# Kernel tuning notes

Hardware: AMD Instinct MI355X
Metric: run time of the kernel (lower is better)

The kernel has to match this reference:

```python
import jax, jax.numpy as jnp
import numpy as np

N = 50000
E = 800000
D_IN = 128
D_OUT = 64


def setup_inputs() -> dict:
    key = jax.random.key(0)
    ks = jax.random.split(key, 8)
    x = jax.random.normal(ks[0], (N, D_IN), dtype=jnp.float32)
    edge_index = jax.random.randint(ks[1], (2, E), 0, N, dtype=jnp.int64)
    s = 1.0 / np.sqrt(D_IN)
    # PyG SAGEConv: lin_l (applied to aggregated neighbors, has bias), lin_r (root, no bias)
    w1_l = jax.random.uniform(ks[2], (D_IN, D_IN), jnp.float32, -s, s)
    b1 = jnp.zeros((D_IN,), jnp.float32)
    w1_r = jax.random.uniform(ks[3], (D_IN, D_IN), jnp.float32, -s, s)
    w2_l = jax.random.uniform(ks[4], (D_IN, D_OUT), jnp.float32, -s, s)
    b2 = jnp.zeros((D_OUT,), jnp.float32)
    w2_r = jax.random.uniform(ks[5], (D_IN, D_OUT), jnp.float32, -s, s)
    return {"x": x, "edge_index": edge_index, "w1_l": w1_l, "b1": b1,
            "w1_r": w1_r, "w2_l": w2_l, "b2": b2, "w2_r": w2_r}


def _sage_conv(x, src, dst, w_l, b_l, w_r):
    # mean-aggregate source features at destination nodes
    msg_sum = jax.ops.segment_sum(x[src], dst, num_segments=N)  # [N, d]
    cnt = jax.ops.segment_sum(jnp.ones((src.shape[0],), x.dtype), dst, num_segments=N)
    mean = msg_sum / jnp.maximum(cnt, 1.0)[:, None]
    out = mean @ w_l + b_l + x @ w_r
    # L2 normalize (normalize=True)
    norm = jnp.linalg.norm(out, axis=-1, keepdims=True)
    return out / jnp.maximum(norm, 1e-12)


def reference(x, edge_index, w1_l, b1, w1_r, w2_l, b2, w2_r):
    src, dst = edge_index[0], edge_index[1]
    h = _sage_conv(x, src, dst, w1_l, b1, w1_r)
    h = _sage_conv(h, src, dst, w2_l, b2, w2_r)
    return h
```

## Files before the change

### kernel.cpp

```cpp
#include <hip/hip_runtime.h>
#include <math.h>

#define NN 50000
#define EE 800000
#define NB 196
#define CAP 6144

typedef __attribute__((ext_vector_type(8))) short bf16x8;
typedef __attribute__((ext_vector_type(16))) float f32x16;
typedef __attribute__((ext_vector_type(4))) unsigned short us4;

__device__ inline unsigned short bf16_rne(float f) {
    union { float f; unsigned u; } a; a.f = f;
    unsigned u = a.u;
    u += 0x7fff + ((u >> 16) & 1);
    return (unsigned short)(u >> 16);
}
__device__ inline float bf16_lo(unsigned v) {
    union { unsigned u; float f; } a; a.u = v << 16;
    return a.f;
}
__device__ inline float bf16_hi(unsigned v) {
    union { unsigned u; float f; } a; a.u = v & 0xffff0000u;
    return a.f;
}

__global__ void prep_all_kernel(const float* __restrict__ w1l, const float* __restrict__ w1r,
                                const float* __restrict__ w2l, const float* __restrict__ w2r,
                                unsigned short* __restrict__ wt1, unsigned short* __restrict__ wt2,
                                unsigned short* __restrict__ y1pad, unsigned short* __restrict__ y2pad,
                                int* __restrict__ bcur) {
    int idx = blockIdx.x * 256 + threadIdx.x;
    if (idx < 32768) {
        int n = idx >> 7, k = idx & 127;
        float v = (n < 128) ? w1l[(size_t)k * 128 + n] : w1r[(size_t)k * 128 + (n - 128)];
        wt1[idx] = bf16_rne(v);
    } else if (idx < 49152) {
        int j = idx - 32768;
        int n = j >> 7, k = j & 127;
        float v = (n < 64) ? w2l[(size_t)k * 64 + n] : w2r[(size_t)k * 64 + (n - 64)];
        wt2[j] = bf16_rne(v);
    } else {
        int j = idx - 49152;
        if (j < 128) y1pad[j] = 0;
        else if (j < 192) y2pad[j - 128] = 0;
        else if (j < 192 + NB) bcur[j - 192] = 0;
    }
}

__global__ __launch_bounds__(1024) void bin_kernel(
        const int* __restrict__ src, const int* __restrict__ dst,
        int* __restrict__ gcur, int* __restrict__ rec, int E) {
    __shared__ int hist[NB];
    __shared__ int cur[NB];
    const int t = threadIdx.x;
    const int per = (E + gridDim.x - 1) / gridDim.x;
    const int lo = blockIdx.x * per;
    const int hi = min(lo + per, E);

    for (int i = t; i < NB; i += 1024) hist[i] = 0;
    __syncthreads();
    for (int e = lo + t; e < hi; e += 1024)
        atomicAdd(&hist[dst[e] >> 8], 1);
    __syncthreads();
    for (int i = t; i < NB; i += 1024)
        cur[i] = atomicAdd(&gcur[i], hist[i]);
    __syncthreads();
    for (int e = lo + t; e < hi; e += 1024) {
        int d = dst[e], s = src[e];
        int cb = d >> 8;
        int p = atomicAdd(&cur[cb], 1);
        if (p < CAP) rec[(size_t)cb * CAP + p] = ((d & 255) << 16) | s;
    }
}

__global__ __launch_bounds__(256) void place_kernel(
        const int* __restrict__ rec, const int* __restrict__ bcur,
        int* __restrict__ rowoff, unsigned short* __restrict__ csr, int n) {
    __shared__ int bscan[256];
    __shared__ int cnt[256];
    __shared__ int cur[256];
    __shared__ unsigned short sorted[CAP];
    const int cb = blockIdx.x, t = threadIdx.x;

    bscan[t] = (t < NB) ? bcur[t] : 0;
    __syncthreads();
    for (int ofs = 1; ofs < 256; ofs <<= 1) {
        int v = bscan[t];
        int a = (t >= ofs) ? bscan[t - ofs] : 0;
        __syncthreads();
        bscan[t] = v + a;
        __syncthreads();
    }
    const int base = (cb == 0) ? 0 : bscan[cb - 1];

    int m = bcur[cb]; if (m > CAP) m = CAP;
    const int* r = rec + (size_t)cb * CAP;

    cnt[t] = 0;
    __syncthreads();
    for (int i = t; i < m; i += 256) atomicAdd(&cnt[r[i] >> 16], 1);
    __syncthreads();
    int orig = cnt[t];
    for (int ofs = 1; ofs < 256; ofs <<= 1) {
        int v = cnt[t];
        int a = (t >= ofs) ? cnt[t - ofs] : 0;
        __syncthreads();
        cnt[t] = v + a;
        __syncthreads();
    }
    int excl = cnt[t] - orig;
    int node = cb * 256 + t;
    if (node < n) rowoff[node] = base + excl;
    if (node == n - 1) rowoff[n] = base + cnt[t];
    cur[t] = excl;
    __syncthreads();
    for (int i = t; i < m; i += 256) {
        int rr = r[i];
        int pos = atomicAdd(&cur[rr >> 16], 1);
        sorted[pos] = (unsigned short)(rr & 0xffff);
    }
    __syncthreads();
    for (int i = t; i < m; i += 256) csr[base + i] = sorted[i];
}

template <int CO, bool BF16IN>
__global__ __launch_bounds__(256) void transform_mfma_kernel(
        const void* __restrict__ xin, const unsigned short* __restrict__ wt,
        const float* __restrict__ bias, unsigned short* __restrict__ ybuf,
        unsigned short* __restrict__ rbuf, int n) {
    constexpr int HALF = CO / 2;
    constexpr int LDW = 136;
    __shared__ unsigned short Xs[64][LDW];
    __shared__ unsigned short Ws[64][LDW];

    const int t = threadIdx.x;
    const int node0 = blockIdx.x * 64;
    const int gy = blockIdx.y;

    if (BF16IN) {
        const unsigned short* xb = (const unsigned short*)xin;
        for (int e = t; e < 64 * 16; e += 256) {
            int nd = e >> 4, c8 = e & 15;
            int node = node0 + nd;
            int4 v = (node < n) ? ((const int4*)(xb + (size_t)node * 128))[c8]
                                : make_int4(0, 0, 0, 0);
            *(int4*)&Xs[nd][c8 * 8] = v;
        }
    } else {
        const float* xf = (const float*)xin;
        for (int e = t; e < 64 * 32; e += 256) {
            int nd = e >> 5, c4 = e & 31;
            int node = node0 + nd;
            float4 v = (node < n) ? ((const float4*)xf)[(size_t)node * 32 + c4]
                                  : make_float4(0.f, 0.f, 0.f, 0.f);
            us4 p;
            p.x = bf16_rne(v.x); p.y = bf16_rne(v.y); p.z = bf16_rne(v.z); p.w = bf16_rne(v.w);
            *(us4*)&Xs[nd][c4 * 4] = p;
        }
    }
    for (int e = t; e < 64 * 16; e += 256) {
        int nd = e >> 4, c8 = e & 15;
        int4 v = ((const int4*)(wt + ((size_t)(gy * 64 + nd)) * 128))[c8];
        *(int4*)&Ws[nd][c8 * 8] = v;
    }
    __syncthreads();

    const int lane = t & 63, wave = t >> 6;
    const int wm = (wave & 1) * 32, wn = (wave >> 1) * 32;
    const int ml = wm + (lane & 31);
    const int nl = wn + (lane & 31);
    const int koff = (lane >> 5) * 8;

    f32x16 acc;
#pragma unroll
    for (int r = 0; r < 16; r++) acc[r] = 0.f;

#pragma unroll
    for (int kk = 0; kk < 8; kk++) {
        bf16x8 a = *(const bf16x8*)&Xs[ml][kk * 16 + koff];
        bf16x8 b = *(const bf16x8*)&Ws[nl][kk * 16 + koff];
        acc = __builtin_amdgcn_mfma_f32_32x32x16_bf16(a, b, acc, 0, 0, 0);
    }

    const int col = gy * 64 + wn + (lane & 31);
    if (col < HALF) {
#pragma unroll
        for (int r = 0; r < 16; r++) {
            int row = (r & 3) + 8 * (r >> 2) + 4 * (lane >> 5);
            int node = node0 + wm + row;
            if (node < n) ybuf[(size_t)node * HALF + col] = bf16_rne(acc[r]);
        }
    } else {
        const float bj = bias[col - HALF];
#pragma unroll
        for (int r = 0; r < 16; r++) {
            int row = (r & 3) + 8 * (r >> 2) + 4 * (lane >> 5);
            int node = node0 + wm + row;
            if (node < n) rbuf[(size_t)node * HALF + (col - HALF)] = bf16_rne(acc[r] + bj);
        }
    }
}

__global__ __launch_bounds__(256) void gather128_kernel(
        const unsigned short* __restrict__ y, const unsigned short* __restrict__ rrb,
        const int* __restrict__ rowoff, const unsigned short* __restrict__ csr,
        unsigned short* __restrict__ out, int n) {
    const int wave = threadIdx.x >> 6;
    const int lane = threadIdx.x & 63;
    const int node = blockIdx.x * 4 + wave;
    if (node >= n) return;
    const int g = lane >> 4;
    const int q = lane & 15;

    const int off = rowoff[node];
    const int end = rowoff[node + 1];
    const int deg = end - off;

    float acc[8];
#pragma unroll
    for (int j = 0; j < 8; j++) acc[j] = 0.f;

    for (int k0 = 0; k0 < deg; k0 += 8) {
        int kk0 = off + k0 + g;
        int kk1 = off + k0 + 4 + g;
        int i0 = (kk0 < end) ? (int)csr[kk0] : n;
        int i1 = (kk1 < end) ? (int)csr[kk1] : n;
        uint4 v0 = *(const uint4*)(y + (size_t)i0 * 128 + q * 8);
        uint4 v1 = *(const uint4*)(y + (size_t)i1 * 128 + q * 8);
        const unsigned* u0 = (const unsigned*)&v0;
        const unsigned* u1 = (const unsigned*)&v1;
#pragma unroll
        for (int i = 0; i < 4; i++) {
            acc[2 * i]     += bf16_lo(u0[i]) + bf16_lo(u1[i]);
            acc[2 * i + 1] += bf16_hi(u0[i]) + bf16_hi(u1[i]);
        }
    }
#pragma unroll
    for (int j = 0; j < 8; j++) {
        acc[j] += __shfl_xor(acc[j], 16, 64);
        acc[j] += __shfl_xor(acc[j], 32, 64);
    }
    const float im = 1.0f / fmaxf((float)deg, 1.0f);
    uint4 rv = *(const uint4*)(rrb + (size_t)node * 128 + q * 8);
    const unsigned* ru = (const unsigned*)&rv;
    float v[8];
    float ss = 0.f;
#pragma unroll
    for (int i = 0; i < 4; i++) {
        v[2 * i]     = acc[2 * i] * im     + bf16_lo(ru[i]);
        v[2 * i + 1] = acc[2 * i + 1] * im + bf16_hi(ru[i]);
    }
#pragma unroll
    for (int j = 0; j < 8; j++) ss += v[j] * v[j];
#pragma unroll
    for (int m = 8; m >= 1; m >>= 1) ss += __shfl_xor(ss, m, 64);
    const float rn = 1.0f / fmaxf(sqrtf(ss), 1e-12f);
    if (g == 0) {
        uint4 pk;
        unsigned* pu = (unsigned*)&pk;
#pragma unroll
        for (int i = 0; i < 4; i++)
            pu[i] = (unsigned)bf16_rne(v[2 * i] * rn) |
                    ((unsigned)bf16_rne(v[2 * i + 1] * rn) << 16);
        *(uint4*)(out + (size_t)node * 128 + q * 8) = pk;
    }
}

__global__ __launch_bounds__(256) void gather64_kernel(
        const unsigned short* __restrict__ y, const unsigned short* __restrict__ rrb,
        const int* __restrict__ rowoff, const unsigned short* __restrict__ csr,
        float* __restrict__ out, int n) {
    const int wave = threadIdx.x >> 6;
    const int lane = threadIdx.x & 63;
    const int node = blockIdx.x * 4 + wave;
    if (node >= n) return;
    const int g = lane >> 3;
    const int q = lane & 7;

    const int off = rowoff[node];
    const int end = rowoff[node + 1];
    const int deg = end - off;

    float acc[8];
#pragma unroll
    for (int j = 0; j < 8; j++) acc[j] = 0.f;

    for (int k0 = 0; k0 < deg; k0 += 16) {
        int kk0 = off + k0 + g;
        int kk1 = off + k0 + 8 + g;
        int i0 = (kk0 < end) ? (int)csr[kk0] : n;
        int i1 = (kk1 < end) ? (int)csr[kk1] : n;
        uint4 v0 = *(const uint4*)(y + (size_t)i0 * 64 + q * 8);
        uint4 v1 = *(const uint4*)(y + (size_t)i1 * 64 + q * 8);
        const unsigned* u0 = (const unsigned*)&v0;
        const unsigned* u1 = (const unsigned*)&v1;
#pragma unroll
        for (int i = 0; i < 4; i++) {
            acc[2 * i]     += bf16_lo(u0[i]) + bf16_lo(u1[i]);
            acc[2 * i + 1] += bf16_hi(u0[i]) + bf16_hi(u1[i]);
        }
    }
#pragma unroll
    for (int j = 0; j < 8; j++) {
        acc[j] += __shfl_xor(acc[j], 8, 64);
        acc[j] += __shfl_xor(acc[j], 16, 64);
        acc[j] += __shfl_xor(acc[j], 32, 64);
    }
    const float im = 1.0f / fmaxf((float)deg, 1.0f);
    uint4 rv = *(const uint4*)(rrb + (size_t)node * 64 + q * 8);
    const unsigned* ru = (const unsigned*)&rv;
    float v[8];
    float ss = 0.f;
#pragma unroll
    for (int i = 0; i < 4; i++) {
        v[2 * i]     = acc[2 * i] * im     + bf16_lo(ru[i]);
        v[2 * i + 1] = acc[2 * i + 1] * im + bf16_hi(ru[i]);
    }
#pragma unroll
    for (int j = 0; j < 8; j++) ss += v[j] * v[j];
#pragma unroll
    for (int m = 4; m >= 1; m >>= 1) ss += __shfl_xor(ss, m, 64);
    const float rn = 1.0f / fmaxf(sqrtf(ss), 1e-12f);
    if (g == 0) {
        float4 o0 = make_float4(v[0] * rn, v[1] * rn, v[2] * rn, v[3] * rn);
        float4 o1 = make_float4(v[4] * rn, v[5] * rn, v[6] * rn, v[7] * rn);
        *(float4*)(out + (size_t)node * 64 + q * 8) = o0;
        *(float4*)(out + (size_t)node * 64 + q * 8 + 4) = o1;
    }
}

extern "C" void kernel_launch(void* const* d_in, const int* in_sizes, int n_in,
                              void* d_out, int out_size, void* d_ws, size_t ws_size,
                              hipStream_t stream) {
    const float* x   = (const float*)d_in[0];
    const int*   ei  = (const int*)d_in[1];
    const float* w1l = (const float*)d_in[2];
    const float* b1  = (const float*)d_in[3];
    const float* w1r = (const float*)d_in[4];
    const float* w2l = (const float*)d_in[5];
    const float* b2  = (const float*)d_in[6];
    const float* w2r = (const float*)d_in[7];
    float* out = (float*)d_out;

    const int* src = ei;
    const int* dst = ei + EE;

    char* ws = (char*)d_ws;
    auto align = [](size_t v) { return (v + 255) & ~(size_t)255; };
    int*   rowoff = (int*)ws;                 size_t o = align((size_t)(NN + 1) * 4);
    int*   bcur   = (int*)(ws + o);           o += align((size_t)NB * 4);
    int*   rec    = (int*)(ws + o);           o += align((size_t)NB * CAP * 4);
    unsigned short* csr = (unsigned short*)(ws + o); o += align((size_t)EE * 2);
    unsigned short* wt1 = (unsigned short*)(ws + o); o += align((size_t)256 * 128 * 2);
    unsigned short* wt2 = (unsigned short*)(ws + o); o += align((size_t)128 * 128 * 2);
    unsigned short* y1  = (unsigned short*)(ws + o); o += align((size_t)(NN + 1) * 128 * 2);
    unsigned short* r1  = (unsigned short*)(ws + o); o += align((size_t)NN * 128 * 2);
    unsigned short* h1  = (unsigned short*)(ws + o); o += align((size_t)NN * 128 * 2);
    unsigned short* y2  = (unsigned short*)(ws + o); o += align((size_t)(NN + 1) * 64 * 2);
    unsigned short* r2  = (unsigned short*)(ws + o); o += align((size_t)NN * 64 * 2);

    prep_all_kernel<<<194, 256, 0, stream>>>(w1l, w1r, w2l, w2r, wt1, wt2,
                                             y1 + (size_t)NN * 128, y2 + (size_t)NN * 64, bcur);
    bin_kernel<<<256, 1024, 0, stream>>>(src, dst, bcur, rec, EE);
    place_kernel<<<NB, 256, 0, stream>>>(rec, bcur, rowoff, csr, NN);

    transform_mfma_kernel<256, false><<<dim3((NN + 63) / 64, 4), 256, 0, stream>>>(
        x, wt1, b1, y1, r1, NN);
    gather128_kernel<<<(NN + 3) / 4, 256, 0, stream>>>(y1, r1, rowoff, csr, h1, NN);

    transform_mfma_kernel<128, true><<<dim3((NN + 63) / 64, 2), 256, 0, stream>>>(
        h1, wt2, b2, y2, r2, NN);
    gather64_kernel<<<(NN + 3) / 4, 256, 0, stream>>>(y2, r2, rowoff, csr, out, NN);
}
```

Baseline: 201.2 us.

## Map one node per lane group in gather kernels with 8-way unrolled loads

Gather kernels now assign a 16-lane (or 8-lane) group per destination node instead of a whole wave, so a wave processes several nodes at once and the cross-group shuffle reduction is removed. Each thread loads 8 neighbor rows per iteration, raising memory-level parallelism. This cuts idle lanes and shuffle work, but adds divergence between nodes of different degree in a wave and padding loads when degree isn't a multiple of 8.

```diff
diff --git a/kernel.cpp b/kernel.cpp
--- a/kernel.cpp
+++ b/kernel.cpp
@@ -206,12 +206,10 @@
         const unsigned short* __restrict__ y, const unsigned short* __restrict__ rrb,
         const int* __restrict__ rowoff, const unsigned short* __restrict__ csr,
         unsigned short* __restrict__ out, int n) {
-    const int wave = threadIdx.x >> 6;
-    const int lane = threadIdx.x & 63;
-    const int node = blockIdx.x * 4 + wave;
+    const int gi = threadIdx.x >> 4;
+    const int q  = threadIdx.x & 15;
+    const int node = blockIdx.x * 16 + gi;
     if (node >= n) return;
-    const int g = lane >> 4;
-    const int q = lane & 15;
 
     const int off = rowoff[node];
     const int end = rowoff[node + 1];
@@ -222,24 +220,25 @@
     for (int j = 0; j < 8; j++) acc[j] = 0.f;
 
     for (int k0 = 0; k0 < deg; k0 += 8) {
-        int kk0 = off + k0 + g;
-        int kk1 = off + k0 + 4 + g;
-        int i0 = (kk0 < end) ? (int)csr[kk0] : n;
-        int i1 = (kk1 < end) ? (int)csr[kk1] : n;
-        uint4 v0 = *(const uint4*)(y + (size_t)i0 * 128 + q * 8);
-        uint4 v1 = *(const uint4*)(y + (size_t)i1 * 128 + q * 8);
-        const unsigned* u0 = (const unsigned*)&v0;
-        const unsigned* u1 = (const unsigned*)&v1;
-#pragma unroll
-        for (int i = 0; i < 4; i++) {
-            acc[2 * i]     += bf16_lo(u0[i]) + bf16_lo(u1[i]);
-            acc[2 * i + 1] += bf16_hi(u0[i]) + bf16_hi(u1[i]);
-        }
-    }
-#pragma unroll
-    for (int j = 0; j < 8; j++) {
-        acc[j] += __shfl_xor(acc[j], 16, 64);
-        acc[j] += __shfl_xor(acc[j], 32, 64);
+        int idx[8];
+#pragma unroll
+        for (int j = 0; j < 8; j++) {
+            int kk = off + k0 + j;
+            idx[j] = (kk < end) ? (int)csr[kk] : n;
+        }
+        uint4 v[8];
+#pragma unroll
+        for (int j = 0; j < 8; j++)
+            v[j] = *(const uint4*)(y + (size_t)idx[j] * 128 + q * 8);
+#pragma unroll
+        for (int j = 0; j < 8; j++) {
+            const unsigned* u = (const unsigned*)&v[j];
+#pragma unroll
+            for (int i = 0; i < 4; i++) {
+                acc[2 * i]     += bf16_lo(u[i]);
+                acc[2 * i + 1] += bf16_hi(u[i]);
+            }
+        }
     }
     const float im = 1.0f / fmaxf((float)deg, 1.0f);
     uint4 rv = *(const uint4*)(rrb + (size_t)node * 128 + q * 8);
@@ -256,27 +255,23 @@
 #pragma unroll
     for (int m = 8; m >= 1; m >>= 1) ss += __shfl_xor(ss, m, 64);
     const float rn = 1.0f / fmaxf(sqrtf(ss), 1e-12f);
-    if (g == 0) {
-        uint4 pk;
-        unsigned* pu = (unsigned*)&pk;
-#pragma unroll
-        for (int i = 0; i < 4; i++)
-            pu[i] = (unsigned)bf16_rne(v[2 * i] * rn) |
-                    ((unsigned)bf16_rne(v[2 * i + 1] * rn) << 16);
-        *(uint4*)(out + (size_t)node * 128 + q * 8) = pk;
-    }
+    uint4 pk;
+    unsigned* pu = (unsigned*)&pk;
+#pragma unroll
+    for (int i = 0; i < 4; i++)
+        pu[i] = (unsigned)bf16_rne(v[2 * i] * rn) |
+                ((unsigned)bf16_rne(v[2 * i + 1] * rn) << 16);
+    *(uint4*)(out + (size_t)node * 128 + q * 8) = pk;
 }
 
 __global__ __launch_bounds__(256) void gather64_kernel(
         const unsigned short* __restrict__ y, const unsigned short* __restrict__ rrb,
         const int* __restrict__ rowoff, const unsigned short* __restrict__ csr,
         float* __restrict__ out, int n) {
-    const int wave = threadIdx.x >> 6;
-    const int lane = threadIdx.x & 63;
-    const int node = blockIdx.x * 4 + wave;
+    const int gi = threadIdx.x >> 3;
+    const int q  = threadIdx.x & 7;
+    const int node = blockIdx.x * 32 + gi;
     if (node >= n) return;
-    const int g = lane >> 3;
-    const int q = lane & 7;
 
     const int off = rowoff[node];
     const int end = rowoff[node + 1];
@@ -286,26 +281,26 @@
 #pragma unroll
     for (int j = 0; j < 8; j++) acc[j] = 0.f;
 
-    for (int k0 = 0; k0 < deg; k0 += 16) {
-        int kk0 = off + k0 + g;
-        int kk1 = off + k0 + 8 + g;
-        int i0 = (kk0 < end) ? (int)csr[kk0] : n;
-        int i1 = (kk1 < end) ? (int)csr[kk1] : n;
-        uint4 v0 = *(const uint4*)(y + (size_t)i0 * 64 + q * 8);
-        uint4 v1 = *(const uint4*)(y + (size_t)i1 * 64 + q * 8);
-        const unsigned* u0 = (const unsigned*)&v0;
-        const unsigned* u1 = (const unsigned*)&v1;
-#pragma unroll
-        for (int i = 0; i < 4; i++) {
-            acc[2 * i]     += bf16_lo(u0[i]) + bf16_lo(u1[i]);
-            acc[2 * i + 1] += bf16_hi(u0[i]) + bf16_hi(u1[i]);
-        }
-    }
-#pragma unroll
-    for (int j = 0; j < 8; j++) {
-        acc[j] += __shfl_xor(acc[j], 8, 64);
-        acc[j] += __shfl_xor(acc[j], 16, 64);
-        acc[j] += __shfl_xor(acc[j], 32, 64);
+    for (int k0 = 0; k0 < deg; k0 += 8) {
+        int idx[8];
+#pragma unroll
+        for (int j = 0; j < 8; j++) {
+            int kk = off + k0 + j;
+            idx[j] = (kk < end) ? (int)csr[kk] : n;
+        }
+        uint4 v[8];
+#pragma unroll
+        for (int j = 0; j < 8; j++)
+            v[j] = *(const uint4*)(y + (size_t)idx[j] * 64 + q * 8);
+#pragma unroll
+        for (int j = 0; j < 8; j++) {
+            const unsigned* u = (const unsigned*)&v[j];
+#pragma unroll
+            for (int i = 0; i < 4; i++) {
+                acc[2 * i]     += bf16_lo(u[i]);
+                acc[2 * i + 1] += bf16_hi(u[i]);
+            }
+        }
     }
     const float im = 1.0f / fmaxf((float)deg, 1.0f);
     uint4 rv = *(const uint4*)(rrb + (size_t)node * 64 + q * 8);
@@ -322,12 +317,10 @@
 #pragma unroll
     for (int m = 4; m >= 1; m >>= 1) ss += __shfl_xor(ss, m, 64);
     const float rn = 1.0f / fmaxf(sqrtf(ss), 1e-12f);
-    if (g == 0) {
-        float4 o0 = make_float4(v[0] * rn, v[1] * rn, v[2] * rn, v[3] * rn);
-        float4 o1 = make_float4(v[4] * rn, v[5] * rn, v[6] * rn, v[7] * rn);
-        *(float4*)(out + (size_t)node * 64 + q * 8) = o0;
-        *(float4*)(out + (size_t)node * 64 + q * 8 + 4) = o1;
-    }
+    float4 o0 = make_float4(v[0] * rn, v[1] * rn, v[2] * rn, v[3] * rn);
+    float4 o1 = make_float4(v[4] * rn, v[5] * rn, v[6] * rn, v[7] * rn);
+    *(float4*)(out + (size_t)node * 64 + q * 8) = o0;
+    *(float4*)(out + (size_t)node * 64 + q * 8 + 4) = o1;
 }
 
 extern "C" void kernel_launch(void* const* d_in, const int* in_sizes, int n_in,
@@ -367,9 +360,9 @@
 
     transform_mfma_kernel<256, false><<<dim3((NN + 63) / 64, 4), 256, 0, stream>>>(
         x, wt1, b1, y1, r1, NN);
-    gather128_kernel<<<(NN + 3) / 4, 256, 0, stream>>>(y1, r1, rowoff, csr, h1, NN);
+    gather128_kernel<<<(NN + 15) / 16, 256, 0, stream>>>(y1, r1, rowoff, csr, h1, NN);
 
     transform_mfma_kernel<128, true><<<dim3((NN + 63) / 64, 2), 256, 0, stream>>>(
         h1, wt2, b2, y2, r2, NN);
-    gather64_kernel<<<(NN + 3) / 4, 256, 0, stream>>>(y2, r2, rowoff, csr, out, NN);
-}
+    gather64_kernel<<<(NN + 31) / 32, 256, 0, stream>>>(y2, r2, rowoff, csr, out, NN);
+}
```

New measurement: 189.6 us. 5.8% less time.
